# Kernel tuning notes

Hardware: AMD Instinct MI355X
Metric: run time of the kernel (lower is better)

## Reference

```python
import jax, jax.numpy as jnp
import numpy as np

B, S, T = 64, 128, 64
V, E, H, L = 32000, 512, 512, 2
PAD, BOS = 0, 1


def setup_inputs() -> dict:
    key = jax.random.key(0)
    ks = jax.random.split(key, 14)
    w = lambda k, shape: (jax.random.normal(k, shape, jnp.float32) * 0.05)
    src_emb = w(ks[0], (V, E)).at[PAD].set(0.0)
    tgt_emb = w(ks[1], (V, E)).at[PAD].set(0.0)
    enc_Wih = w(ks[2], (L, 4 * H, E))
    enc_Whh = w(ks[3], (L, 4 * H, H))
    enc_b = w(ks[4], (L, 4 * H))          # b_ih + b_hh fused
    dec_Wih = w(ks[5], (L, 4 * H, E))
    dec_Whh = w(ks[6], (L, 4 * H, H))
    dec_b = w(ks[7], (L, 4 * H))
    gen_W = w(ks[8], (V, H))
    gen_b = jnp.zeros((V,), jnp.float32)
    x_seqs = jax.random.randint(ks[9], (B, S), 0, V, jnp.int32)
    x_len = jnp.sort(jax.random.randint(ks[10], (B,), 1, S + 1, jnp.int32))[::-1]
    y_seqs = jax.random.randint(ks[11], (B, T), 0, V, jnp.int32)
    teacher = jax.random.randint(ks[12], (T - 1,), 0, 2, jnp.int32)
    return dict(x_seqs=x_seqs, x_len=x_len, y_seqs=y_seqs, teacher=teacher,
                src_emb=src_emb, tgt_emb=tgt_emb,
                enc_Wih=enc_Wih, enc_Whh=enc_Whh, enc_b=enc_b,
                dec_Wih=dec_Wih, dec_Whh=dec_Whh, dec_b=dec_b,
                gen_W=gen_W, gen_b=gen_b)


def lstm_cell(x, h, c, Wih, Whh, b):
    # torch gate order: i, f, g, o
    g = x @ Wih.T + h @ Whh.T + b
    i, f, gg, o = jnp.split(g, 4, axis=-1)
    c2 = jax.nn.sigmoid(f) * c + jax.nn.sigmoid(i) * jnp.tanh(gg)
    h2 = jax.nn.sigmoid(o) * jnp.tanh(c2)
    return h2, c2


def encode(x_seqs, x_len, src_emb, Wih, Whh, b):
    emb = src_emb[x_seqs]                                  # [B,S,E]
    mask = jnp.arange(S)[None, :] < x_len[:, None]         # [B,S] valid steps
    inp = emb.transpose(1, 0, 2)                           # [S,B,E]
    m_t = mask.T                                           # [S,B]
    hs, cs = [], []
    for l in range(L):
        def step(carry, xs, l=l):
            h, c = carry
            xt, m = xs
            h2, c2 = lstm_cell(xt, h, c, Wih[l], Whh[l], b[l])
            m = m[:, None]
            h2 = jnp.where(m, h2, h)   # freeze state past sequence length
            c2 = jnp.where(m, c2, c)
            return (h2, c2), h2
        z = jnp.zeros((B, H), inp.dtype)
        (hT, cT), out = jax.lax.scan(step, (z, z), (inp, m_t))
        inp = out
        hs.append(hT)
        cs.append(cT)
    return jnp.stack(hs), jnp.stack(cs)                    # each [L,B,H]


def reference(x_seqs, x_len, y_seqs, teacher, src_emb, tgt_emb,
              enc_Wih, enc_Whh, enc_b, dec_Wih, dec_Whh, dec_b, gen_W, gen_b):
    h0, c0 = encode(x_seqs, x_len, src_emb, enc_Wih, enc_Whh, enc_b)

    def step(carry, xs):
        h, c, inp = carry                                  # [L,B,H],[L,B,H],[B]
        y_t, tf = xs                                       # [B], scalar flag
        x = tgt_emb[inp]                                   # [B,E]
        new_h, new_c = [], []
        for l in range(L):
            hl, cl = lstm_cell(x, h[l], c[l], dec_Wih[l], dec_Whh[l], dec_b[l])
            new_h.append(hl); new_c.append(cl)
            x = hl
        logp = jax.nn.log_softmax(x @ gen_W.T + gen_b, axis=-1)   # [B,V]
        expct = jnp.take_along_axis(logp, y_t[:, None], axis=1)[:, 0]
        pred = jnp.argmax(logp, axis=1).astype(inp.dtype)
        nxt = jnp.where(tf > 0, y_t, pred)                 # scheduled sampling
        return (jnp.stack(new_h), jnp.stack(new_c), nxt), expct

    inp0 = jnp.full((B,), BOS, jnp.int32)
    _, outp = jax.lax.scan(step, (h0, c0, inp0), (y_seqs[:, 1:].T, teacher))
    return outp.T                                          # [B, T-1]
```

## Files before the change

### kernel.cpp

```cpp
#include <hip/hip_runtime.h>
#include <hip/hip_bf16.h>
#include <cstdint>
#include <cstddef>

namespace {

constexpr int B = 64, S = 128, T = 64, V = 32000, E = 512, H = 512;
constexpr int G4 = 2048;
constexpr int TM1 = T - 1;
constexpr int CHUNK = 32;
constexpr int BH = B * H;
constexpr int NT = 128;
constexpr int NTILES = V / NT;
constexpr float MARGIN = 0.02f;
constexpr unsigned NBLK = 256;

typedef __attribute__((ext_vector_type(8))) short short8v;
typedef __attribute__((ext_vector_type(4))) float f32x4;

struct GemmSh { float As[16][68]; float Bs[16][132]; };
struct StepSh { float gs[64][17]; };
struct GenSh  { float lds[64][NT + 4]; float pv1[64][4], pv2[64][4], psum[64][4], mrow[64];
                int pi1[64][4], pi2[64][4]; };
struct RedSh  { float sM[256], sS[256], red[256]; float cV[16], rV[16]; int cI[16]; int cN, nxt; };

__device__ __forceinline__ float sigf(float x) { return 1.0f / (1.0f + expf(-x)); }

__device__ __forceinline__ void split3(float w, __hip_bfloat16& a, __hip_bfloat16& b,
                                       __hip_bfloat16& c2) {
    a = __float2bfloat16(w);
    float r = w - __bfloat162float(a);
    b = __float2bfloat16(r);
    c2 = __float2bfloat16(r - __bfloat162float(b));
}

__device__ __forceinline__ unsigned ld_coh_u32(const unsigned* p) {
    unsigned v;
    asm volatile("global_load_dword %0, %1, off sc0 sc1\n\ts_waitcnt vmcnt(0)"
                 : "=v"(v) : "v"(p) : "memory");
    return v;
}
__device__ __forceinline__ void st_coh_u32(unsigned* p, unsigned v) {
    asm volatile("global_store_dword %0, %1, off sc0 sc1" :: "v"(p), "v"(v) : "memory");
}
__device__ __forceinline__ float ld_coh_f32(const float* p) {
    float v;
    asm volatile("global_load_dword %0, %1, off sc0 sc1\n\ts_waitcnt vmcnt(0)"
                 : "=v"(v) : "v"(p));
    return v;
}
__device__ __forceinline__ void st_coh_f32(float* p, float v) {
    asm volatile("global_store_dword %0, %1, off sc0 sc1" :: "v"(p), "v"(v));
}
__device__ __forceinline__ f32x4 ld_coh_f32x4(const float* p) {
    f32x4 v;
    asm volatile("global_load_dwordx4 %0, %1, off sc0 sc1\n\ts_waitcnt vmcnt(0)"
                 : "=v"(v) : "v"(p));
    return v;
}
__device__ __forceinline__ void st_coh_b16(__hip_bfloat16* p, __hip_bfloat16 v) {
    unsigned short us; __builtin_memcpy(&us, &v, 2);
    unsigned u = us;
    asm volatile("global_store_short %0, %1, off sc0 sc1" :: "v"(p), "v"(u));
}
__device__ __forceinline__ void st_coh_b128(__hip_bfloat16* p, short8v v) {
    asm volatile("global_store_dwordx4 %0, %1, off sc0 sc1" :: "v"(p), "v"(v));
}
__device__ __forceinline__ void fence_vm() {
    asm volatile("s_waitcnt vmcnt(0)" ::: "memory");
}

__device__ __forceinline__ void issue12_nw(const __hip_bfloat16* p0, const __hip_bfloat16* p1,
                                           const __hip_bfloat16* p2, short8v* q)
{
    asm volatile(
        "global_load_dwordx4 %0, %12, off sc0 sc1\n\t"
        "global_load_dwordx4 %1, %12, off offset:64 sc0 sc1\n\t"
        "global_load_dwordx4 %2, %12, off offset:128 sc0 sc1\n\t"
        "global_load_dwordx4 %3, %12, off offset:192 sc0 sc1\n\t"
        "global_load_dwordx4 %4, %13, off sc0 sc1\n\t"
        "global_load_dwordx4 %5, %13, off offset:64 sc0 sc1\n\t"
        "global_load_dwordx4 %6, %13, off offset:128 sc0 sc1\n\t"
        "global_load_dwordx4 %7, %13, off offset:192 sc0 sc1\n\t"
        "global_load_dwordx4 %8, %14, off sc0 sc1\n\t"
        "global_load_dwordx4 %9, %14, off offset:64 sc0 sc1\n\t"
        "global_load_dwordx4 %10, %14, off offset:128 sc0 sc1\n\t"
        "global_load_dwordx4 %11, %14, off offset:192 sc0 sc1"
        : "=&v"(q[0]), "=&v"(q[1]), "=&v"(q[2]), "=&v"(q[3]),
          "=&v"(q[4]), "=&v"(q[5]), "=&v"(q[6]), "=&v"(q[7]),
          "=&v"(q[8]), "=&v"(q[9]), "=&v"(q[10]), "=&v"(q[11])
        : "v"(p0), "v"(p1), "v"(p2));
}
__device__ __forceinline__ void issue12_w12(const __hip_bfloat16* p0, const __hip_bfloat16* p1,
                                            const __hip_bfloat16* p2, short8v* q)
{
    asm volatile(
        "global_load_dwordx4 %0, %12, off sc0 sc1\n\t"
        "global_load_dwordx4 %1, %12, off offset:64 sc0 sc1\n\t"
        "global_load_dwordx4 %2, %12, off offset:128 sc0 sc1\n\t"
        "global_load_dwordx4 %3, %12, off offset:192 sc0 sc1\n\t"
        "global_load_dwordx4 %4, %13, off sc0 sc1\n\t"
        "global_load_dwordx4 %5, %13, off offset:64 sc0 sc1\n\t"
        "global_load_dwordx4 %6, %13, off offset:128 sc0 sc1\n\t"
        "global_load_dwordx4 %7, %13, off offset:192 sc0 sc1\n\t"
        "global_load_dwordx4 %8, %14, off sc0 sc1\n\t"
        "global_load_dwordx4 %9, %14, off offset:64 sc0 sc1\n\t"
        "global_load_dwordx4 %10, %14, off offset:128 sc0 sc1\n\t"
        "global_load_dwordx4 %11, %14, off offset:192 sc0 sc1\n\t"
        "s_waitcnt vmcnt(12)"
        : "=&v"(q[0]), "=&v"(q[1]), "=&v"(q[2]), "=&v"(q[3]),
          "=&v"(q[4]), "=&v"(q[5]), "=&v"(q[6]), "=&v"(q[7]),
          "=&v"(q[8]), "=&v"(q[9]), "=&v"(q[10]), "=&v"(q[11])
        : "v"(p0), "v"(p1), "v"(p2) : "memory");
}
__device__ __forceinline__ void wait_vm0_fence() {
    asm volatile("s_waitcnt vmcnt(0)" ::: "memory");
    __builtin_amdgcn_sched_barrier(0);
}

__device__ __forceinline__ void ldg16(const __hip_bfloat16* p0, const __hip_bfloat16* p1,
                                      const __hip_bfloat16* p2, const __hip_bfloat16* p3,
                                      short8v* q)
{
    asm volatile(
        "global_load_dwordx4 %0, %16, off sc0 sc1\n\t"
        "global_load_dwordx4 %1, %16, off offset:64 sc0 sc1\n\t"
        "global_load_dwordx4 %2, %16, off offset:128 sc0 sc1\n\t"
        "global_load_dwordx4 %3, %16, off offset:192 sc0 sc1\n\t"
        "global_load_dwordx4 %4, %17, off sc0 sc1\n\t"
        "global_load_dwordx4 %5, %17, off offset:64 sc0 sc1\n\t"
        "global_load_dwordx4 %6, %17, off offset:128 sc0 sc1\n\t"
        "global_load_dwordx4 %7, %17, off offset:192 sc0 sc1\n\t"
        "global_load_dwordx4 %8, %18, off sc0 sc1\n\t"
        "global_load_dwordx4 %9, %18, off offset:64 sc0 sc1\n\t"
        "global_load_dwordx4 %10, %18, off offset:128 sc0 sc1\n\t"
        "global_load_dwordx4 %11, %18, off offset:192 sc0 sc1\n\t"
        "global_load_dwordx4 %12, %19, off sc0 sc1\n\t"
        "global_load_dwordx4 %13, %19, off offset:64 sc0 sc1\n\t"
        "global_load_dwordx4 %14, %19, off offset:128 sc0 sc1\n\t"
        "global_load_dwordx4 %15, %19, off offset:192 sc0 sc1\n\t"
        "s_waitcnt vmcnt(0)"
        : "=&v"(q[0]), "=&v"(q[1]), "=&v"(q[2]), "=&v"(q[3]),
          "=&v"(q[4]), "=&v"(q[5]), "=&v"(q[6]), "=&v"(q[7]),
          "=&v"(q[8]), "=&v"(q[9]), "=&v"(q[10]), "=&v"(q[11]),
          "=&v"(q[12]), "=&v"(q[13]), "=&v"(q[14]), "=&v"(q[15])
        : "v"(p0), "v"(p1), "v"(p2), "v"(p3));
}

__device__ __forceinline__ void ldg8(const __hip_bfloat16* p0, const __hip_bfloat16* p1,
                                     short8v* q)
{
    asm volatile(
        "global_load_dwordx4 %0, %8, off sc0 sc1\n\t"
        "global_load_dwordx4 %1, %8, off offset:64 sc0 sc1\n\t"
        "global_load_dwordx4 %2, %8, off offset:128 sc0 sc1\n\t"
        "global_load_dwordx4 %3, %8, off offset:192 sc0 sc1\n\t"
        "global_load_dwordx4 %4, %9, off sc0 sc1\n\t"
        "global_load_dwordx4 %5, %9, off offset:64 sc0 sc1\n\t"
        "global_load_dwordx4 %6, %9, off offset:128 sc0 sc1\n\t"
        "global_load_dwordx4 %7, %9, off offset:192 sc0 sc1\n\t"
        "s_waitcnt vmcnt(0)"
        : "=&v"(q[0]), "=&v"(q[1]), "=&v"(q[2]), "=&v"(q[3]),
          "=&v"(q[4]), "=&v"(q[5]), "=&v"(q[6]), "=&v"(q[7])
        : "v"(p0), "v"(p1));
}

__device__ __forceinline__ void gbar(unsigned* flags, unsigned* rel, unsigned& ep)
{
    unsigned tgt = ++ep;
    fence_vm();
    __syncthreads();
    const int tid = threadIdx.x;
    if (blockIdx.x == 0) {
        if (tid > 0) {
            int spins = 0;
            while (ld_coh_u32(&flags[tid * 32]) < tgt) {
                if (spins < 8) __builtin_amdgcn_s_sleep(1);
                else           __builtin_amdgcn_s_sleep(32);
                if (++spins > (1 << 16)) break;
            }
        }
        __syncthreads();
        st_coh_u32(&rel[tid * 32], tgt);
    } else {
        if (tid == 0) {
            st_coh_u32(&flags[blockIdx.x * 32], tgt);
            int spins = 0;
            while (ld_coh_u32(&rel[blockIdx.x * 32]) < tgt) {
                if (spins < 8) __builtin_amdgcn_s_sleep(1);
                else           __builtin_amdgcn_s_sleep(32);
                if (++spins > (1 << 16)) break;
            }
        }
        __syncthreads();
    }
}

__global__ __launch_bounds__(256)
void split_dec_k(const float* __restrict__ Wih, const float* __restrict__ Whh,
                 const float* __restrict__ bsrc,
                 __hip_bfloat16* __restrict__ P0, __hip_bfloat16* __restrict__ P1,
                 __hip_bfloat16* __restrict__ P2, float* __restrict__ bint)
{
    int row = blockIdx.x;
    int l = row >> 11, jp = row & 2047;
    int kh = jp >> 2, g = jp & 3, src = g * 512 + kh;
    const float* wih = Wih + ((size_t)l * 2048 + src) * 512;
    const float* whh = Whh + ((size_t)l * 2048 + src) * 512;
    size_t ro = (size_t)row * 1024;
    for (int k = threadIdx.x; k < 1024; k += 256) {
        float w = (k < 512) ? whh[k] : wih[k - 512];
        __hip_bfloat16 a, b, c2; split3(w, a, b, c2);
        P0[ro + k] = a; P1[ro + k] = b; P2[ro + k] = c2;
    }
    if (threadIdx.x == 0) bint[row] = bsrc[l * 2048 + src];
}

__global__ __launch_bounds__(256)
void split_enc_k(const float* __restrict__ Whh,
                 __hip_bfloat16* __restrict__ P0, __hip_bfloat16* __restrict__ P1,
                 __hip_bfloat16* __restrict__ P2)
{
    int row = blockIdx.x;
    int kh = row >> 2, g = row & 3, src = g * 512 + kh;
    const float* whh = Whh + (size_t)src * 512;
    size_t ro = (size_t)row * 512;
    for (int k = threadIdx.x; k < 512; k += 256) {
        __hip_bfloat16 a, b, c2; split3(whh[k], a, b, c2);
        P0[ro + k] = a; P1[ro + k] = b; P2[ro + k] = c2;
    }
}

__device__ void gemm_tile(char* shraw, const float* __restrict__ A,
                          const float* __restrict__ Wt, const float* __restrict__ bias,
                          float* __restrict__ C,
                          const int* __restrict__ xseq, int m0, int bx, int by)
{
    GemmSh* sh = reinterpret_cast<GemmSh*>(shraw);
    constexpr int K = 512, BK = 16;
    int tid = threadIdx.x;
    int bm = by * 64, bn = bx * 128;
    int tx = tid & 15, ty = tid >> 4;
    float acc[4][8] = {};

    int lm = tid >> 2, lk = (tid & 3) << 2;
    const float* Arow;
    {
        int mg = m0 + bm + lm; int tt = mg >> 6, b = mg & 63;
        Arow = A + (size_t)xseq[b * S + tt] * K;
    }
    int ln = tid >> 1, lkb = (tid & 1) << 3;
    const float* Brow = Wt + (size_t)(bn + ln) * K;

    for (int k0 = 0; k0 < K; k0 += BK) {
        float4 av = *(const float4*)(Arow + k0 + lk);
        sh->As[lk + 0][lm] = av.x; sh->As[lk + 1][lm] = av.y;
        sh->As[lk + 2][lm] = av.z; sh->As[lk + 3][lm] = av.w;
        float4 bv0 = *(const float4*)(Brow + k0 + lkb);
        float4 bv1 = *(const float4*)(Brow + k0 + lkb + 4);
        sh->Bs[lkb + 0][ln] = bv0.x; sh->Bs[lkb + 1][ln] = bv0.y;
        sh->Bs[lkb + 2][ln] = bv0.z; sh->Bs[lkb + 3][ln] = bv0.w;
        sh->Bs[lkb + 4][ln] = bv1.x; sh->Bs[lkb + 5][ln] = bv1.y;
        sh->Bs[lkb + 6][ln] = bv1.z; sh->Bs[lkb + 7][ln] = bv1.w;
        __syncthreads();
#pragma unroll
        for (int kk = 0; kk < BK; ++kk) {
            const float4 a4  = *(const float4*)&sh->As[kk][ty * 4];
            const float4 b4a = *(const float4*)&sh->Bs[kk][tx * 8];
            const float4 b4b = *(const float4*)&sh->Bs[kk][tx * 8 + 4];
            const float a[4]  = {a4.x, a4.y, a4.z, a4.w};
            const float bb[8] = {b4a.x, b4a.y, b4a.z, b4a.w,
                                 b4b.x, b4b.y, b4b.z, b4b.w};
#pragma unroll
            for (int i = 0; i < 4; ++i)
#pragma unroll
                for (int j = 0; j < 8; ++j)
                    acc[i][j] = fmaf(a[i], bb[j], acc[i][j]);
        }
        __syncthreads();
    }
#pragma unroll
    for (int i = 0; i < 4; ++i) {
        size_t crow = (size_t)(bm + ty * 4 + i) * G4;
#pragma unroll
        for (int j = 0; j < 8; ++j) {
            int cg = bn + tx * 8 + j;
            int jp = ((cg & 511) << 2) | (cg >> 9);
            st_coh_f32(C + crow + jp, acc[i][j] + bias[cg]);
        }
    }
}

template<int KHALF, bool ADDXC, bool MASK>
__device__ void step_body(char* shraw, int blk,
    const __hip_bfloat16* __restrict__ hA0, const __hip_bfloat16* __restrict__ hA1,
    const __hip_bfloat16* __restrict__ hA2,
    const __hip_bfloat16* __restrict__ xA0, const __hip_bfloat16* __restrict__ xA1,
    const __hip_bfloat16* __restrict__ xA2,
    const __hip_bfloat16* __restrict__ W0, const __hip_bfloat16* __restrict__ W1,
    const __hip_bfloat16* __restrict__ W2,
    const float* __restrict__ addsrc, const float* __restrict__ h_in,
    float* __restrict__ h_out, float* __restrict__ c,
    __hip_bfloat16* __restrict__ o0, __hip_bfloat16* __restrict__ o1,
    __hip_bfloat16* __restrict__ o2,
    const int* __restrict__ x_len, int t)
{
    StepSh* sh = reinterpret_cast<StepSh*>(shraw);
    int tid = threadIdx.x;
    int wave = tid >> 6, lane = tid & 63;
    int lr = lane & 15, kg = (lane >> 4) * 8;
    int arow = wave * 16 + lr;
    int brow = blk * 16 + lr;
    const int KW = 512 * KHALF;
    constexpr int NG = KHALF * 4;

    f32x4 acc0 = {0,0,0,0}, acc1 = {0,0,0,0}, acc2 = {0,0,0,0};
    const size_t aoff = (size_t)arow * 512 + kg;
    const size_t boff = (size_t)brow * KW + kg;

    auto ap = [&](int g, int pl) -> const __hip_bfloat16* {
        const __hip_bfloat16* base;
        if (KHALF == 2 && g >= 4) {
            base = (pl == 0) ? xA0 : (pl == 1) ? xA1 : xA2;
            return base + aoff + (size_t)(g - 4) * 128;
        }
        base = (pl == 0) ? hA0 : (pl == 1) ? hA1 : hA2;
        return base + aoff + (size_t)g * 128;
    };

    short8v q[2][12];
    issue12_nw(ap(0, 0), ap(0, 1), ap(0, 2), q[0]);
#pragma unroll
    for (int g = 0; g < NG; ++g) {
        if (g + 1 < NG) {
            issue12_w12(ap(g + 1, 0), ap(g + 1, 1), ap(g + 1, 2), q[(g + 1) & 1]);
            __builtin_amdgcn_sched_barrier(0);
        } else {
            wait_vm0_fence();
        }
#pragma unroll
        for (int j = 0; j < 4; ++j) {
            int k0 = g * 128 + j * 32;
            short8v b0 = *(const short8v*)(W0 + boff + k0);
            short8v b1 = *(const short8v*)(W1 + boff + k0);
            short8v b2 = *(const short8v*)(W2 + boff + k0);
            short8v a0 = q[g & 1][j], a1 = q[g & 1][4 + j], a2 = q[g & 1][8 + j];
            acc0 = __builtin_amdgcn_mfma_f32_16x16x32_bf16(a0, b0, acc0, 0, 0, 0);
            acc1 = __builtin_amdgcn_mfma_f32_16x16x32_bf16(a0, b1, acc1, 0, 0, 0);
            acc2 = __builtin_amdgcn_mfma_f32_16x16x32_bf16(a1, b0, acc2, 0, 0, 0);
            acc0 = __builtin_amdgcn_mfma_f32_16x16x32_bf16(a1, b1, acc0, 0, 0, 0);
            acc1 = __builtin_amdgcn_mfma_f32_16x16x32_bf16(a0, b2, acc1, 0, 0, 0);
            acc2 = __builtin_amdgcn_mfma_f32_16x16x32_bf16(a2, b0, acc2, 0, 0, 0);
        }
    }
    int rb = (lane >> 4) * 4;
#pragma unroll
    for (int r = 0; r < 4; ++r)
        sh->gs[wave * 16 + rb + r][lr] = acc0[r] + acc1[r] + acc2[r];
    __syncthreads();

    int b = tid >> 2, khl = tid & 3;
    int khg = blk * 4 + khl;
    f32x4 add;
    if (ADDXC) add = ld_coh_f32x4(addsrc + (size_t)b * G4 + (size_t)khg * 4);
    else       add = *(const f32x4*)(addsrc + (size_t)khg * 4);
    float gi = sh->gs[b][khl * 4 + 0] + add[0];
    float gf = sh->gs[b][khl * 4 + 1] + add[1];
    float gg = sh->gs[b][khl * 4 + 2] + add[2];
    float go2 = sh->gs[b][khl * 4 + 3] + add[3];
    size_t idx = (size_t)b * H + khg;
    float cold = ld_coh_f32(c + idx);
    float c2 = sigf(gf) * cold + sigf(gi) * tanhf(gg);
    float h2 = sigf(go2) * tanhf(c2);
    if (MASK) {
        bool mk = t < x_len[b];
        if (!mk) { h2 = ld_coh_f32(h_in + idx); c2 = cold; }
    }
    if (h_out) st_coh_f32(h_out + idx, h2);
    st_coh_f32(c + idx, c2);
    __hip_bfloat16 s0, s1, s2; split3(h2, s0, s1, s2);
    st_coh_b16(o0 + idx, s0); st_coh_b16(o1 + idx, s1); st_coh_b16(o2 + idx, s2);
}

__device__ void gen_body(char* shraw, int bid,
                         const __hip_bfloat16* __restrict__ hbf,
                         const __hip_bfloat16* __restrict__ Wbf,
                         const float* __restrict__ genb,
                         float* __restrict__ part)
{
    GenSh* sh = reinterpret_cast<GenSh*>(shraw);
    int tid = threadIdx.x;
    int wave = tid >> 6, lane = tid & 63;
    int n0 = bid * NT;
    int lr = lane & 15;
    int kg = (lane >> 4) * 8;

    f32x4 acc[4][2];
    const f32x4 zero = {0.f, 0.f, 0.f, 0.f};
#pragma unroll
    for (int i = 0; i < 4; ++i)
#pragma unroll
        for (int j = 0; j < 2; ++j) acc[i][j] = zero;

    const __hip_bfloat16* Arow = hbf + (size_t)lr * 512 + kg;
    const __hip_bfloat16* Brow = Wbf + (size_t)(n0 + wave * 32 + lr) * 512 + kg;
#pragma unroll
    for (int g = 0; g < 4; ++g) {
        short8v qa[16], qb[8];
        ldg16(Arow + g * 128, Arow + 8192 + g * 128,
              Arow + 16384 + g * 128, Arow + 24576 + g * 128, qa);
        ldg8(Brow + g * 128, Brow + 8192 + g * 128, qb);
#pragma unroll
        for (int j = 0; j < 4; ++j) {
#pragma unroll
            for (int mf = 0; mf < 4; ++mf)
#pragma unroll
                for (int nf = 0; nf < 2; ++nf)
                    acc[mf][nf] = __builtin_amdgcn_mfma_f32_16x16x32_bf16(
                        qa[mf * 4 + j], qb[nf * 4 + j], acc[mf][nf], 0, 0, 0);
        }
    }
#pragma unroll
    for (int nf = 0; nf < 2; ++nf) {
        int colLocal = wave * 32 + nf * 16 + lr;
        float bias = genb[n0 + colLocal];
#pragma unroll
        for (int mf = 0; mf < 4; ++mf) {
#pragma unroll
            for (int r = 0; r < 4; ++r) {
                int row = mf * 16 + (lane >> 4) * 4 + r;
                sh->lds[row][colLocal] = acc[mf][nf][r] + bias;
            }
        }
    }
    __syncthreads();

    int row = tid >> 2, q = tid & 3;
    int cbase = q * 32;
    float v1 = -3.4e38f, v2 = -3.4e38f; int i1 = 0x7fffffff, i2 = 0x7fffffff;
    for (int c = 0; c < 32; ++c) {
        float v = sh->lds[row][cbase + c];
        int ci = cbase + c;
        if (v > v1 || (v == v1 && ci < i1)) { v2 = v1; i2 = i1; v1 = v; i1 = ci; }
        else if (v > v2 || (v == v2 && ci < i2)) { v2 = v; i2 = ci; }
    }
    sh->pv1[row][q] = v1; sh->pi1[row][q] = i1; sh->pv2[row][q] = v2; sh->pi2[row][q] = i2;
    __syncthreads();

    float t1 = -3.4e38f, t2 = -3.4e38f; int j1 = 0x7fffffff, j2 = 0x7fffffff;
    if (q == 0) {
        for (int k = 0; k < 4; ++k) {
            float a1 = sh->pv1[row][k]; int a1i = sh->pi1[row][k];
            float a2 = sh->pv2[row][k]; int a2i = sh->pi2[row][k];
            if (a1 > t1 || (a1 == t1 && a1i < j1)) { t2 = t1; j2 = j1; t1 = a1; j1 = a1i; }
            else if (a1 > t2 || (a1 == t2 && a1i < j2)) { t2 = a1; j2 = a1i; }
            if (a2 > t1 || (a2 == t1 && a2i < j1)) { t2 = t1; j2 = j1; t1 = a2; j1 = a2i; }
            else if (a2 > t2 || (a2 == t2 && a2i < j2)) { t2 = a2; j2 = a2i; }
        }
        sh->mrow[row] = t1;
    }
    __syncthreads();
    float m = sh->mrow[row];
    float s = 0.f;
    for (int c = 0; c < 32; ++c) s += expf(sh->lds[row][cbase + c] - m);
    sh->psum[row][q] = s;
    __syncthreads();
    if (q == 0) {
        float sum = sh->psum[row][0] + sh->psum[row][1] + sh->psum[row][2] + sh->psum[row][3];
        float* p = part + ((size_t)bid * B + row) * 6;
        st_coh_f32(p + 0, t1);
        st_coh_f32(p + 1, t2);
        st_coh_u32((unsigned*)(p + 2), (unsigned)(n0 + j1));
        st_coh_u32((unsigned*)(p + 3), (unsigned)(n0 + j2));
        st_coh_f32(p + 4, sum);
    }
}

__device__ void reduce_body(char* shraw, int b,
                            const float* __restrict__ part,
                            const float* __restrict__ h,
                            const float* __restrict__ genW, const float* __restrict__ genb,
                            const float* __restrict__ tgt_emb,
                            const int* __restrict__ y_seqs, const int* __restrict__ teacher,
                            float* __restrict__ outp,
                            __hip_bfloat16* __restrict__ xp0, __hip_bfloat16* __restrict__ xp1,
                            __hip_bfloat16* __restrict__ xp2, int t)
{
    RedSh* sh = reinterpret_cast<RedSh*>(shraw);
    int tid = threadIdx.x;
    int y = y_seqs[b * T + t + 1];
    const float* hrow = h + (size_t)b * 512;
    float h_a = ld_coh_f32(hrow + tid);
    float h_b = ld_coh_f32(hrow + tid + 256);

    float p_top1 = -3.4e38f, p_top2 = -3.4e38f, p_sum = 0.f;
    int p_i1 = 0x7fffffff, p_i2 = 0x7fffffff;
    if (tid < NTILES) {
        const float* p = part + ((size_t)tid * B + b) * 6;
        f32x4 v4 = ld_coh_f32x4(p);
        p_top1 = v4[0]; p_top2 = v4[1];
        p_i1 = __float_as_int(v4[2]);
        p_i2 = __float_as_int(v4[3]);
        p_sum = ld_coh_f32(p + 4);
    }
    sh->sM[tid] = p_top1; __syncthreads();
    for (int o = 128; o; o >>= 1) { if (tid < o) sh->sM[tid] = fmaxf(sh->sM[tid], sh->sM[tid + o]); __syncthreads(); }
    float M = sh->sM[0];
    if (tid == 0) sh->cN = 0;
    __syncthreads();

    float Ssum = (tid < NTILES) ? p_sum * expf(p_top1 - M) : 0.f;
    if (tid < NTILES) {
        if (p_top1 >= M - MARGIN) { int j = atomicAdd(&sh->cN, 1); if (j < 16) { sh->cV[j] = p_top1; sh->cI[j] = p_i1; } }
        if (p_top2 >= M - MARGIN) { int j = atomicAdd(&sh->cN, 1); if (j < 16) { sh->cV[j] = p_top2; sh->cI[j] = p_i2; } }
    }
    sh->sS[tid] = Ssum; __syncthreads();
    for (int o = 128; o; o >>= 1) { if (tid < o) sh->sS[tid] += sh->sS[tid + o]; __syncthreads(); }
    float lse = M + logf(sh->sS[0]);
    int nc = sh->cN < 16 ? sh->cN : 16;

    {
        const float* wrow = genW + (size_t)y * 512;
        float s = fmaf(h_a, wrow[tid], 0.f) + h_b * wrow[tid + 256];
        sh->red[tid] = s; __syncthreads();
        for (int o = 128; o; o >>= 1) { if (tid < o) sh->red[tid] += sh->red[tid + o]; __syncthreads(); }
        if (tid == 0) outp[b * TM1 + t] = sh->red[0] + genb[y] - lse;
        __syncthreads();
    }
    if (nc > 1) {
        for (int j = 0; j < nc; ++j) {
            const float* wrow = genW + (size_t)sh->cI[j] * 512;
            float s = fmaf(h_a, wrow[tid], 0.f) + h_b * wrow[tid + 256];
            sh->red[tid] = s; __syncthreads();
            for (int o = 128; o; o >>= 1) { if (tid < o) sh->red[tid] += sh->red[tid + o]; __syncthreads(); }
            if (tid == 0) sh->rV[j] = sh->red[0] + genb[sh->cI[j]];
            __syncthreads();
        }
    }
    if (tid == 0) {
        int winner;
        if (nc == 1) winner = sh->cI[0];
        else {
            float bv = -3.4e38f; int bi = 0x7fffffff;
            for (int j = 0; j < nc; ++j)
                if (sh->rV[j] > bv || (sh->rV[j] == bv && sh->cI[j] < bi)) { bv = sh->rV[j]; bi = sh->cI[j]; }
            winner = bi;
        }
        sh->nxt = (teacher[t] > 0) ? y : winner;
    }
    __syncthreads();
    int tok = sh->nxt;
    for (int k = tid; k < 512; k += 256) {
        float w = tgt_emb[(size_t)tok * 512 + k];
        __hip_bfloat16 s0, s1, s2; split3(w, s0, s1, s2);
        st_coh_b16(xp0 + (size_t)b * 512 + k, s0);
        st_coh_b16(xp1 + (size_t)b * 512 + k, s1);
        st_coh_b16(xp2 + (size_t)b * 512 + k, s2);
    }
}

struct Args {
    const int *x_seqs, *x_len, *y_seqs, *teacher;
    const float *src_emb, *tgt_emb, *eWih, *eb, *genW, *genb;
    float* Xc;
    const __hip_bfloat16 *eP0, *eP1, *eP2;
    const __hip_bfloat16 *e1P0, *e1P1, *e1P2;
    const float* ebint;
    const __hip_bfloat16 *dP0, *dP1, *dP2;
    const float* bint;
    float *hf32, *cbuf, *dech1;
    __hip_bfloat16 *P, *xP, *Wbf;
    float* part;
    float* outp;
    unsigned *flags, *rel;
};

__global__ __launch_bounds__(256, 1)
void persist_k(Args a)
{
    __shared__ __align__(16) char shpool[40960];
    unsigned ep = 0;
    const int bid = blockIdx.x;
    const int tid = threadIdx.x;
    const int gtid = bid * 256 + tid;
    const int GS = NBLK * 256;

    auto Pl = [&](int l, int slot, int pl) {
        return a.P + (((size_t)(l * 2 + slot)) * 3 + pl) * BH; };

    for (int i = gtid; i < BH; i += GS) {
        st_coh_f32(a.hf32 + i, 0.f); st_coh_f32(a.hf32 + 2 * BH + i, 0.f);
        st_coh_f32(a.cbuf + i, 0.f); st_coh_f32(a.cbuf + BH + i, 0.f);
    }
    {
        unsigned* p0 = (unsigned*)Pl(0, 0, 0);
        unsigned* p1 = (unsigned*)Pl(1, 0, 0);
        for (int i = gtid; i < 3 * BH / 2; i += GS) { st_coh_u32(p0 + i, 0u); st_coh_u32(p1 + i, 0u); }
    }
    gbar(a.flags, a.rel, ep);

    for (int c0 = 0; c0 < S; c0 += CHUNK) {
        for (int tile = bid; tile < 512; tile += NBLK)
            gemm_tile(shpool, a.src_emb, a.eWih, a.eb, a.Xc,
                      a.x_seqs, c0 * B, tile & 15, tile >> 4);
        gbar(a.flags, a.rel, ep);
        for (int tl = 0; tl < CHUNK; ++tl) {
            int t = c0 + tl;
            if (bid < 128) {
                step_body<1, true, true>(shpool, bid,
                    Pl(0, t & 1, 0), Pl(0, t & 1, 1), Pl(0, t & 1, 2),
                    nullptr, nullptr, nullptr,
                    a.eP0, a.eP1, a.eP2,
                    a.Xc + (size_t)tl * B * G4,
                    a.hf32 + (size_t)(t & 1) * BH, a.hf32 + (size_t)((t + 1) & 1) * BH,
                    a.cbuf,
                    Pl(0, (t + 1) & 1, 0), Pl(0, (t + 1) & 1, 1), Pl(0, (t + 1) & 1, 2),
                    a.x_len, t);
            } else if (t >= 1) {
                int u = t - 1;
                step_body<2, false, true>(shpool, bid - 128,
                    Pl(1, u & 1, 0), Pl(1, u & 1, 1), Pl(1, u & 1, 2),
                    Pl(0, t & 1, 0), Pl(0, t & 1, 1), Pl(0, t & 1, 2),
                    a.e1P0, a.e1P1, a.e1P2,
                    a.ebint,
                    a.hf32 + (size_t)(2 + (u & 1)) * BH, a.hf32 + (size_t)(2 + ((u + 1) & 1)) * BH,
                    a.cbuf + BH,
                    Pl(1, (u + 1) & 1, 0), Pl(1, (u + 1) & 1, 1), Pl(1, (u + 1) & 1, 2),
                    a.x_len, u);
            }
            gbar(a.flags, a.rel, ep);
        }
    }
    if (bid < 128) {
        int u = S - 1;
        step_body<2, false, true>(shpool, bid,
            Pl(1, u & 1, 0), Pl(1, u & 1, 1), Pl(1, u & 1, 2),
            Pl(0, (u + 1) & 1, 0), Pl(0, (u + 1) & 1, 1), Pl(0, (u + 1) & 1, 2),
            a.e1P0, a.e1P1, a.e1P2,
            a.ebint,
            a.hf32 + (size_t)(2 + (u & 1)) * BH, a.hf32 + (size_t)(2 + ((u + 1) & 1)) * BH,
            a.cbuf + BH,
            Pl(1, (u + 1) & 1, 0), Pl(1, (u + 1) & 1, 1), Pl(1, (u + 1) & 1, 2),
            a.x_len, u);
    }
    gbar(a.flags, a.rel, ep);

    {
        const int N8 = V * E / 8;
        for (int i = gtid; i < N8; i += GS) {
            float4 x = *(const float4*)(a.genW + (size_t)i * 8);
            float4 y = *(const float4*)(a.genW + (size_t)i * 8 + 4);
            __hip_bfloat16 tmp[8];
            tmp[0] = __float2bfloat16(x.x); tmp[1] = __float2bfloat16(x.y);
            tmp[2] = __float2bfloat16(x.z); tmp[3] = __float2bfloat16(x.w);
            tmp[4] = __float2bfloat16(y.x); tmp[5] = __float2bfloat16(y.y);
            tmp[6] = __float2bfloat16(y.z); tmp[7] = __float2bfloat16(y.w);
            st_coh_b128(a.Wbf + (size_t)i * 8, *(const short8v*)tmp);
        }
        for (int i = gtid; i < BH; i += GS) {
            int k = i & 511;
            float w = a.tgt_emb[512 + k];
            __hip_bfloat16 s0, s1, s2; split3(w, s0, s1, s2);
            st_coh_b16(a.xP + i, s0);
            st_coh_b16(a.xP + BH + i, s1);
            st_coh_b16(a.xP + 2 * BH + i, s2);
        }
    }
    gbar(a.flags, a.rel, ep);

    for (int t = 0; t < TM1; ++t) {
        int si = t & 1, so = si ^ 1;
        if (bid < 128)
            step_body<2, false, false>(shpool, bid,
                Pl(0, si, 0), Pl(0, si, 1), Pl(0, si, 2),
                a.xP, a.xP + BH, a.xP + 2 * BH,
                a.dP0, a.dP1, a.dP2, a.bint,
                nullptr, nullptr, a.cbuf,
                Pl(0, so, 0), Pl(0, so, 1), Pl(0, so, 2),
                nullptr, 0);
        gbar(a.flags, a.rel, ep);
        if (bid < 128)
            step_body<2, false, false>(shpool, bid,
                Pl(1, si, 0), Pl(1, si, 1), Pl(1, si, 2),
                Pl(0, so, 0), Pl(0, so, 1), Pl(0, so, 2),
                a.dP0 + (size_t)G4 * 1024, a.dP1 + (size_t)G4 * 1024,
                a.dP2 + (size_t)G4 * 1024, a.bint + G4,
                nullptr, a.dech1, a.cbuf + BH,
                Pl(1, so, 0), Pl(1, so, 1), Pl(1, so, 2),
                nullptr, 0);
        gbar(a.flags, a.rel, ep);
        if (bid < NTILES)
            gen_body(shpool, bid, Pl(1, so, 0), a.Wbf, a.genb, a.part);
        gbar(a.flags, a.rel, ep);
        if (bid < B)
            reduce_body(shpool, bid, a.part, a.dech1, a.genW, a.genb, a.tgt_emb,
                        a.y_seqs, a.teacher, a.outp,
                        a.xP, a.xP + BH, a.xP + 2 * BH, t);
        gbar(a.flags, a.rel, ep);
    }
}

}

extern "C" void kernel_launch(void* const* d_in, const int* in_sizes, int n_in,
                              void* d_out, int out_size, void* d_ws, size_t ws_size,
                              hipStream_t stream)
{
    (void)in_sizes; (void)n_in; (void)out_size;
    const int*   x_seqs  = (const int*)  d_in[0];
    const int*   x_len   = (const int*)  d_in[1];
    const int*   y_seqs  = (const int*)  d_in[2];
    const int*   teacher = (const int*)  d_in[3];
    const float* src_emb = (const float*)d_in[4];
    const float* tgt_emb = (const float*)d_in[5];
    const float* eWih    = (const float*)d_in[6];
    const float* eWhh    = (const float*)d_in[7];
    const float* eb      = (const float*)d_in[8];
    const float* dWih    = (const float*)d_in[9];
    const float* dWhh    = (const float*)d_in[10];
    const float* db      = (const float*)d_in[11];
    const float* genW    = (const float*)d_in[12];
    const float* genb    = (const float*)d_in[13];

    float* w = (float*)d_ws;
    size_t off = 0;
    auto take = [&](size_t n) { float* p = w + off; off += n; return p; };
    auto takeb = [&](size_t n) { return (__hip_bfloat16*)take((n + 1) / 2); };

    unsigned* flags = (unsigned*)take(256 * 32);
    unsigned* rel   = (unsigned*)take(256 * 32);
    float* Xc = take((size_t)CHUNK * B * G4);
    __hip_bfloat16* eP0  = takeb((size_t)G4 * 512);
    __hip_bfloat16* eP1  = takeb((size_t)G4 * 512);
    __hip_bfloat16* eP2  = takeb((size_t)G4 * 512);
    __hip_bfloat16* e1P0 = takeb((size_t)G4 * 1024);
    __hip_bfloat16* e1P1 = takeb((size_t)G4 * 1024);
    __hip_bfloat16* e1P2 = takeb((size_t)G4 * 1024);
    float* ebint = take((size_t)G4);
    __hip_bfloat16* dP0 = takeb((size_t)2 * G4 * 1024);
    __hip_bfloat16* dP1 = takeb((size_t)2 * G4 * 1024);
    __hip_bfloat16* dP2 = takeb((size_t)2 * G4 * 1024);
    float* bint  = take(2 * (size_t)G4);
    float* hf32  = take(4 * (size_t)BH);
    float* cbuf  = take(2 * (size_t)BH);
    float* dech1 = take((size_t)BH);
    __hip_bfloat16* P  = takeb((size_t)12 * BH);
    __hip_bfloat16* xP = takeb((size_t)3 * BH);
    float* part_f = take((size_t)NTILES * B * 6);
    if (ws_size < off * sizeof(float)) return;

    dim3 tpb256(256);
    split_enc_k<<<dim3(G4), tpb256, 0, stream>>>(eWhh, eP0, eP1, eP2);
    split_dec_k<<<dim3(G4), tpb256, 0, stream>>>(
        eWih + (size_t)G4 * E, eWhh + (size_t)G4 * E, eb + G4, e1P0, e1P1, e1P2, ebint);
    split_dec_k<<<dim3(2 * G4), tpb256, 0, stream>>>(
        dWih, dWhh, db, dP0, dP1, dP2, bint);
    hipError_t _e = hipMemsetAsync(flags, 0, 2 * 256 * 32 * sizeof(unsigned), stream);
    (void)_e;

    Args a;
    a.x_seqs = x_seqs; a.x_len = x_len; a.y_seqs = y_seqs; a.teacher = teacher;
    a.src_emb = src_emb; a.tgt_emb = tgt_emb; a.eWih = eWih; a.eb = eb;
    a.genW = genW; a.genb = genb;
    a.Xc = Xc;
    a.eP0 = eP0; a.eP1 = eP1; a.eP2 = eP2;
    a.e1P0 = e1P0; a.e1P1 = e1P1; a.e1P2 = e1P2; a.ebint = ebint;
    a.dP0 = dP0; a.dP1 = dP1; a.dP2 = dP2; a.bint = bint;
    a.hf32 = hf32; a.cbuf = cbuf; a.dech1 = dech1;
    a.P = P; a.xP = xP;
    a.Wbf = (__hip_bfloat16*)Xc;
    a.part = part_f;
    a.outp = (float*)d_out;
    a.flags = flags; a.rel = rel;

    persist_k<<<dim3(NBLK), tpb256, 0, stream>>>(a);
}
```

Baseline: 10.24 ms.

## Busy-wait in grid barrier, non-temporal generator weight loads, separate Wbf buffer

The grid-barrier spin loops now burn ALU with a chain of dependent FMAs instead of s_sleep, which should cut wake-up latency, and the spin limit is raised. The generator's bf16 weight loads switch from coherent sc0 sc1 to non-temporal loads. Wbf gets its own workspace allocation instead of aliasing the Xc buffer, which uses more memory and may change which data is valid. Busy spinning adds power and issue pressure on CUs shared with working waves.

```diff
diff --git a/kernel.cpp b/kernel.cpp
--- a/kernel.cpp
+++ b/kernel.cpp
@@ -68,6 +68,14 @@
 }
 __device__ __forceinline__ void fence_vm() {
     asm volatile("s_waitcnt vmcnt(0)" ::: "memory");
+}
+
+__device__ __forceinline__ void pause_busy() {
+    float x = 1.0f;
+#pragma unroll
+    for (int i = 0; i < 48; ++i)
+        asm volatile("v_fmac_f32 %0, %1, %1" : "+v"(x) : "v"(1.0000001f));
+    asm volatile("" :: "v"(x));
 }
 
 __device__ __forceinline__ void issue12_nw(const __hip_bfloat16* p0, const __hip_bfloat16* p1,
@@ -147,18 +155,18 @@
         : "v"(p0), "v"(p1), "v"(p2), "v"(p3));
 }
 
-__device__ __forceinline__ void ldg8(const __hip_bfloat16* p0, const __hip_bfloat16* p1,
-                                     short8v* q)
+__device__ __forceinline__ void ldg8_nt(const __hip_bfloat16* p0, const __hip_bfloat16* p1,
+                                        short8v* q)
 {
     asm volatile(
-        "global_load_dwordx4 %0, %8, off sc0 sc1\n\t"
-        "global_load_dwordx4 %1, %8, off offset:64 sc0 sc1\n\t"
-        "global_load_dwordx4 %2, %8, off offset:128 sc0 sc1\n\t"
-        "global_load_dwordx4 %3, %8, off offset:192 sc0 sc1\n\t"
-        "global_load_dwordx4 %4, %9, off sc0 sc1\n\t"
-        "global_load_dwordx4 %5, %9, off offset:64 sc0 sc1\n\t"
-        "global_load_dwordx4 %6, %9, off offset:128 sc0 sc1\n\t"
-        "global_load_dwordx4 %7, %9, off offset:192 sc0 sc1\n\t"
+        "global_load_dwordx4 %0, %8, off nt\n\t"
+        "global_load_dwordx4 %1, %8, off offset:64 nt\n\t"
+        "global_load_dwordx4 %2, %8, off offset:128 nt\n\t"
+        "global_load_dwordx4 %3, %8, off offset:192 nt\n\t"
+        "global_load_dwordx4 %4, %9, off nt\n\t"
+        "global_load_dwordx4 %5, %9, off offset:64 nt\n\t"
+        "global_load_dwordx4 %6, %9, off offset:128 nt\n\t"
+        "global_load_dwordx4 %7, %9, off offset:192 nt\n\t"
         "s_waitcnt vmcnt(0)"
         : "=&v"(q[0]), "=&v"(q[1]), "=&v"(q[2]), "=&v"(q[3]),
           "=&v"(q[4]), "=&v"(q[5]), "=&v"(q[6]), "=&v"(q[7])
@@ -175,9 +183,8 @@
         if (tid > 0) {
             int spins = 0;
             while (ld_coh_u32(&flags[tid * 32]) < tgt) {
-                if (spins < 8) __builtin_amdgcn_s_sleep(1);
-                else           __builtin_amdgcn_s_sleep(32);
-                if (++spins > (1 << 16)) break;
+                pause_busy();
+                if (++spins > (1 << 18)) break;
             }
         }
         __syncthreads();
@@ -187,9 +194,8 @@
             st_coh_u32(&flags[blockIdx.x * 32], tgt);
             int spins = 0;
             while (ld_coh_u32(&rel[blockIdx.x * 32]) < tgt) {
-                if (spins < 8) __builtin_amdgcn_s_sleep(1);
-                else           __builtin_amdgcn_s_sleep(32);
-                if (++spins > (1 << 16)) break;
+                pause_busy();
+                if (++spins > (1 << 18)) break;
             }
         }
         __syncthreads();
@@ -409,7 +415,7 @@
         short8v qa[16], qb[8];
         ldg16(Arow + g * 128, Arow + 8192 + g * 128,
               Arow + 16384 + g * 128, Arow + 24576 + g * 128, qa);
-        ldg8(Brow + g * 128, Brow + 8192 + g * 128, qb);
+        ldg8_nt(Brow + g * 128, Brow + 8192 + g * 128, qb);
 #pragma unroll
         for (int j = 0; j < 4; ++j) {
 #pragma unroll
@@ -747,6 +753,7 @@
     __hip_bfloat16* P  = takeb((size_t)12 * BH);
     __hip_bfloat16* xP = takeb((size_t)3 * BH);
     float* part_f = take((size_t)NTILES * B * 6);
+    __hip_bfloat16* Wbf = takeb((size_t)V * E);
     if (ws_size < off * sizeof(float)) return;
 
     dim3 tpb256(256);
@@ -768,7 +775,7 @@
     a.dP0 = dP0; a.dP1 = dP1; a.dP2 = dP2; a.bint = bint;
     a.hf32 = hf32; a.cbuf = cbuf; a.dech1 = dech1;
     a.P = P; a.xP = xP;
-    a.Wbf = (__hip_bfloat16*)Xc;
+    a.Wbf = Wbf;
     a.part = part_f;
     a.outp = (float*)d_out;
     a.flags = flags; a.rel = rel;
```

New measurement: 10.11 ms. Within noise of the previous version (-1.3%).
